# Kernel optimization log

Hardware: AMD Instinct MI355X
Metric: run time of the kernel (lower is better)

The kernel has to match this reference:

```python
import jax, jax.numpy as jnp
import numpy as np
import math

B, L, D = 4, 2048, 1024        # batch, x_len, x_dim
QKV, H = 64, 16                # qkv_dim, head_dim (number of heads)


def setup_inputs() -> dict:
    key = jax.random.key(0)
    ks = jax.random.split(key, 10)
    s = 1.0 / math.sqrt(D)
    return {
        "x": jax.random.normal(ks[0], (B, L, D), jnp.float32),
        "encoder_x": jax.random.normal(ks[1], (B, L, D), jnp.float32),
        "Wq": jax.random.normal(ks[2], (D, QKV * H), jnp.float32) * s,
        "bq": jax.random.normal(ks[3], (QKV * H,), jnp.float32) * 0.01,
        "Wk": jax.random.normal(ks[4], (D, QKV * H), jnp.float32) * s,
        "bk": jax.random.normal(ks[5], (QKV * H,), jnp.float32) * 0.01,
        "Wv": jax.random.normal(ks[6], (D, QKV * H), jnp.float32) * s,
        "bv": jax.random.normal(ks[7], (QKV * H,), jnp.float32) * 0.01,
        "Wo": jax.random.normal(ks[8], (QKV * H, D), jnp.float32) * s,
        "bo": jax.random.normal(ks[9], (D,), jnp.float32) * 0.01,
    }


def reference(x, encoder_x, Wq, bq, Wk, bk, Wv, bv, Wo, bo):
    # q,k from encoder_x; v from x  -> [B, L, H, QKV]
    q = (encoder_x @ Wq + bq).reshape(B, L, H, QKV)
    k = (encoder_x @ Wk + bk).reshape(B, L, H, QKV)
    v = (x @ Wv + bv).reshape(B, L, H, QKV)
    # explicit [B,H,L,L] score matrix + softmax over k (faithful to source)
    scores = jax.nn.softmax(
        jnp.einsum("bqhd,bkhd->bhqk", q, k) / math.sqrt(QKV), axis=-1
    )
    # faithful to source einsum 'bvhd,bhqk->bvhd': no shared contraction
    # index, so scores are summed over (q,k) and broadcast onto v per (b,h).
    attn = jnp.einsum("bvhd,bhqk->bvhd", v, scores).reshape(B, L, H * QKV)
    return attn @ Wo + bo
```

## Files before the change

### kernel.cpp

```cpp
#include <hip/hip_runtime.h>
#include <stdint.h>


typedef __attribute__((ext_vector_type(8))) short bf16x8;
typedef __attribute__((ext_vector_type(4))) float f32x4;

typedef __attribute__((address_space(1))) void as1_void;
typedef __attribute__((address_space(3))) void as3_void;
#define GLD16(g, s)                                                          \
  __builtin_amdgcn_global_load_lds((as1_void*)(g), (as3_void*)(s), 16, 0, 0)

__device__ __forceinline__ short f2bf(float f) {
  union { float f; uint32_t u; } v; v.f = f;
  uint32_t r = v.u + 0x7FFFu + ((v.u >> 16) & 1u);
  return (short)(r >> 16);
}

__device__ __forceinline__ bf16x8 pack8(f32x4 a, f32x4 b) {
  union { f32x4 f; uint32_t u[4]; } x, y;
  x.f = a; y.f = b;
#pragma unroll
  for (int t = 0; t < 4; ++t) x.u[t] += 0x8000u;
#pragma unroll
  for (int t = 0; t < 4; ++t) y.u[t] += 0x8000u;
  union { bf16x8 v; uint32_t u[4]; } o;
  o.u[0] = __builtin_amdgcn_perm(x.u[1], x.u[0], 0x07060302);
  o.u[1] = __builtin_amdgcn_perm(x.u[3], x.u[2], 0x07060302);
  o.u[2] = __builtin_amdgcn_perm(y.u[1], y.u[0], 0x07060302);
  o.u[3] = __builtin_amdgcn_perm(y.u[3], y.u[2], 0x07060302);
  return o.v;
}

__global__ __launch_bounds__(256) void mid(
    const float* __restrict__ Wo, const float* __restrict__ Wv,
    const float* __restrict__ bv, const float* __restrict__ bo,
    const float* __restrict__ x, short* __restrict__ x_bf,
    short* __restrict__ Wt, float* __restrict__ biasc) {
  constexpr int BK = 64, NW = 1024;
  __shared__ __align__(16) float Bsf[64 * BK];
  __shared__ __align__(16) float Ts[64 * 36];
  const int b = blockIdx.x, tid = threadIdx.x;

  if (b >= 576) {
    const int i = (b - 576) * 256 + tid;
    const float4* p = (const float4*)x;
    float4 a = p[2 * (size_t)i], c = p[2 * (size_t)i + 1];
    *(bf16x8*)(x_bf + 8 * (size_t)i) =
        pack8((f32x4){a.x, a.y, a.z, a.w}, (f32x4){c.x, c.y, c.z, c.w});
    return;
  }

  if (b >= 512) {
    float* red = Bsf;
    const int b3 = b - 512;
    const int nx = tid & 15, ky = tid >> 4;
    const int n = b3 * 16 + nx;
    float s = 0.f;
    for (int k = ky; k < 1024; k += 16)
      s += bv[k] * Wo[(size_t)k * NW + n];
    red[tid] = s;
    __syncthreads();
#pragma unroll
    for (int st = 128; st >= 16; st >>= 1) {
      if (tid < st) red[tid] += red[tid + st];
      __syncthreads();
    }
    if (ky == 0) biasc[n] = 2048.0f * red[nx] + bo[n];
    return;
  }

  const int lane = tid & 63, wave = tid >> 6;
  const int bm = (b >> 4) * 32, bn = (b & 15) * 64;
  const int wm = (wave & 1) * 16, wn = (wave >> 1) * 32;
  const int l15 = lane & 15, quad = lane >> 4;

  f32x4 acc[2];
  acc[0] = (f32x4){0.f, 0.f, 0.f, 0.f};
  acc[1] = (f32x4){0.f, 0.f, 0.f, 0.f};

  const int br = tid >> 4, bc4 = (tid & 15) ^ (br & 7);
  const float* pb = Wv + (size_t)(bn + br) * NW + bc4 * 4;
  float* lb = Bsf + tid * 4;

  const int ajr = tid >> 3, ac4 = (tid & 7) * 4;
  const float* pa = Wo + (size_t)ajr * NW + bm + ac4;

  for (int kt = 0; kt < 1024; kt += BK) {
    float4 va = *(const float4*)(pa);
    float4 vb = *(const float4*)(pa + 32 * (size_t)NW);
    pa += (size_t)BK * NW;
#pragma unroll
    for (int s = 0; s < 4; ++s) GLD16(pb + (size_t)(16 * s) * NW, lb + 1024 * s);
    pb += BK;
    *(float4*)(Ts + ajr * 36 + ac4) = va;
    *(float4*)(Ts + (ajr + 32) * 36 + ac4) = vb;
    __syncthreads();
#pragma unroll
    for (int kk = 0; kk < 2; ++kk) {
      const float* tsp = Ts + ((kk * 4 + quad) * 8) * 36 + wm + l15;
      float av[8];
#pragma unroll
      for (int e = 0; e < 8; ++e) av[e] = tsp[e * 36];
      bf16x8 af = pack8((f32x4){av[0], av[1], av[2], av[3]},
                        (f32x4){av[4], av[5], av[6], av[7]});
#pragma unroll
      for (int j = 0; j < 2; ++j) {
        const int rn = wn + j * 16 + l15;
        const int c4 = kk * 8 + quad * 2;
        f32x4 u0 = *(const f32x4*)(Bsf + (rn * 16 + (c4 ^ (rn & 7))) * 4);
        f32x4 u1 = *(const f32x4*)(Bsf + (rn * 16 + ((c4 + 1) ^ (rn & 7))) * 4);
        acc[j] = __builtin_amdgcn_mfma_f32_16x16x32_bf16(af, pack8(u0, u1),
                                                         acc[j], 0, 0, 0);
      }
    }
    __syncthreads();
  }
#pragma unroll
  for (int j = 0; j < 2; ++j) {
    const int col = bn + wn + j * 16 + l15;
    const int row0 = bm + wm + quad * 4;
#pragma unroll
    for (int r = 0; r < 4; ++r)
      Wt[(size_t)(row0 + r) * NW + col] = f2bf(2048.f * acc[j][r]);
  }
}

__global__ __launch_bounds__(256) void gemm_main(
    const short* __restrict__ A, const short* __restrict__ Bt,
    const float* __restrict__ bias, float* __restrict__ Out,
    int M, int N, int K) {
  constexpr int BK = 64;
  __shared__ __align__(16) char smem[65536];
  short* As0 = (short*)smem;
  short* Bs0 = (short*)(smem + 16384);
  short* As1 = (short*)(smem + 32768);
  short* Bs1 = (short*)(smem + 49152);
  const int tid = threadIdx.x, lane = tid & 63, wave = tid >> 6;
  const int b = blockIdx.x;
  const int bm = (b & 63) * 128;
  const int bn = (b >> 6) * 128;
  const int wm = (wave & 1) * 64, wn = (wave >> 1) * 64;
  const int l15 = lane & 15, quad = lane >> 4;

  f32x4 acc[4][4];
#pragma unroll
  for (int i = 0; i < 4; ++i)
#pragma unroll
    for (int j = 0; j < 4; ++j) acc[i][j] = (f32x4){0.f, 0.f, 0.f, 0.f};

  const int srow = tid >> 3, sc8 = (tid & 7) ^ (srow & 7);
  const short* pa = A + (size_t)(bm + srow) * K + sc8 * 8;
  const short* pb = Bt + (size_t)(bn + srow) * K + sc8 * 8;

#define STAGE(Asx, Bsx, kt)                                                  \
  {                                                                          \
    _Pragma("unroll") for (int s = 0; s < 4; ++s)                            \
        GLD16(pa + (size_t)(32 * s) * K + (kt), (Asx) + tid * 8 + 2048 * s); \
    _Pragma("unroll") for (int s = 0; s < 4; ++s)                            \
        GLD16(pb + (size_t)(32 * s) * K + (kt), (Bsx) + tid * 8 + 2048 * s); \
  }
#define COMPUTE(Asx, Bsx)                                                    \
  {                                                                          \
    _Pragma("unroll") for (int kk = 0; kk < 2; ++kk) {                       \
      bf16x8 af[4], bfr[4];                                                  \
      _Pragma("unroll") for (int i = 0; i < 4; ++i) {                        \
        const int r = wm + i * 16 + l15;                                     \
        af[i] = *(const bf16x8*)((Asx) + r * BK +                            \
                                 ((kk * 4 + quad) ^ (r & 7)) * 8);           \
      }                                                                      \
      _Pragma("unroll") for (int j = 0; j < 4; ++j) {                        \
        const int r = wn + j * 16 + l15;                                     \
        bfr[j] = *(const bf16x8*)((Bsx) + r * BK +                           \
                                  ((kk * 4 + quad) ^ (r & 7)) * 8);          \
      }                                                                      \
      _Pragma("unroll") for (int i = 0; i < 4; ++i)                          \
          _Pragma("unroll") for (int j = 0; j < 4; ++j)                      \
              acc[i][j] = __builtin_amdgcn_mfma_f32_16x16x32_bf16(           \
                  af[i], bfr[j], acc[i][j], 0, 0, 0);                        \
    }                                                                        \
  }

  STAGE(As0, Bs0, 0);
  __syncthreads();

  for (int trip = 0; trip < 8; ++trip) {
    const int kt_e = trip * 128;
    STAGE(As1, Bs1, kt_e + 64);
    COMPUTE(As0, Bs0);
    __syncthreads();
    if (trip < 7) {
      STAGE(As0, Bs0, kt_e + 128);
      COMPUTE(As1, Bs1);
      __syncthreads();
    } else {
      COMPUTE(As1, Bs1);
    }
  }
#undef STAGE
#undef COMPUTE

  float* T = (float*)smem + wave * 1088;
#pragma unroll
  for (int i = 0; i < 4; ++i) {
#pragma unroll
    for (int j = 0; j < 4; ++j) {
      const float bb = bias[bn + wn + j * 16 + l15];
#pragma unroll
      for (int r = 0; r < 4; ++r)
        T[(quad * 4 + r) * 68 + j * 16 + l15] = acc[i][j][r] + bb;
    }
#pragma unroll
    for (int p = 0; p < 4; ++p) {
      const int row = (lane >> 4) + 4 * p;
      const int ch = lane & 15;
      f32x4 v = *(const f32x4*)(T + row * 68 + ch * 4);
      *(f32x4*)(Out + (size_t)(bm + wm + i * 16 + row) * N + bn + wn +
                ch * 4) = v;
    }
  }
}

extern "C" void kernel_launch(void* const* d_in, const int* in_sizes, int n_in,
                              void* d_out, int out_size, void* d_ws,
                              size_t ws_size, hipStream_t stream) {
  const float* x  = (const float*)d_in[0];
  const float* Wv = (const float*)d_in[6];
  const float* bv = (const float*)d_in[7];
  const float* Wo = (const float*)d_in[8];
  const float* bo = (const float*)d_in[9];
  float* out = (float*)d_out;

  constexpr int D = 1024, NO = 1024;
  constexpr int M = 8192;

  char* ws = (char*)d_ws;
  short* x_bf  = (short*)(ws);
  short* wt_bf = (short*)(ws + (16u << 20));
  float* biasc = (float*)(ws + (18u << 20));

  mid<<<4672, 256, 0, stream>>>(Wo, Wv, bv, bo, x, x_bf, wt_bf, biasc);
  gemm_main<<<(M / 128) * (NO / 128), 256, 0, stream>>>(
      x_bf, wt_bf, biasc, out, M, NO, D);
}
```

Before: 153.9 us.

## Double-buffer LDS tiles in Wo·Wv precompute kernel to overlap loads with MFMA

The mid kernel's K-loop that forms the folded Wo·Wv weight now uses two LDS buffers for both operand tiles. The next tile's global loads and LDS stores are issued before the current tile's MFMA compute, and one barrier per step replaces two. This aims to hide global-load latency behind compute, at the cost of doubled LDS usage, which may reduce occupancy.

```diff
diff --git a/kernel.cpp b/kernel.cpp
--- a/kernel.cpp
+++ b/kernel.cpp
@@ -37,8 +37,10 @@
     const float* __restrict__ x, short* __restrict__ x_bf,
     short* __restrict__ Wt, float* __restrict__ biasc) {
   constexpr int BK = 64, NW = 1024;
-  __shared__ __align__(16) float Bsf[64 * BK];
-  __shared__ __align__(16) float Ts[64 * 36];
+  __shared__ __align__(16) float Bsf0[64 * BK];
+  __shared__ __align__(16) float Bsf1[64 * BK];
+  __shared__ __align__(16) float Ts0[64 * 36];
+  __shared__ __align__(16) float Ts1[64 * 36];
   const int b = blockIdx.x, tid = threadIdx.x;
 
   if (b >= 576) {
@@ -51,7 +53,7 @@
   }
 
   if (b >= 512) {
-    float* red = Bsf;
+    float* red = Bsf0;
     const int b3 = b - 512;
     const int nx = tid & 15, ky = tid >> 4;
     const int n = b3 * 16 + nx;
@@ -80,41 +82,57 @@
 
   const int br = tid >> 4, bc4 = (tid & 15) ^ (br & 7);
   const float* pb = Wv + (size_t)(bn + br) * NW + bc4 * 4;
-  float* lb = Bsf + tid * 4;
-
   const int ajr = tid >> 3, ac4 = (tid & 7) * 4;
   const float* pa = Wo + (size_t)ajr * NW + bm + ac4;
 
-  for (int kt = 0; kt < 1024; kt += BK) {
-    float4 va = *(const float4*)(pa);
-    float4 vb = *(const float4*)(pa + 32 * (size_t)NW);
-    pa += (size_t)BK * NW;
-#pragma unroll
-    for (int s = 0; s < 4; ++s) GLD16(pb + (size_t)(16 * s) * NW, lb + 1024 * s);
-    pb += BK;
-    *(float4*)(Ts + ajr * 36 + ac4) = va;
-    *(float4*)(Ts + (ajr + 32) * 36 + ac4) = vb;
+#define STAGEW(Tsx, Bsx, kt)                                                 \
+  {                                                                          \
+    float4 va = *(const float4*)(pa + (size_t)(kt)*NW);                      \
+    float4 vb = *(const float4*)(pa + (size_t)((kt) + 32) * NW);             \
+    _Pragma("unroll") for (int s = 0; s < 4; ++s)                            \
+        GLD16(pb + (size_t)(16 * s) * NW + (kt), (Bsx) + tid * 4 + 1024 * s);\
+    *(float4*)((Tsx) + ajr * 36 + ac4) = va;                                 \
+    *(float4*)((Tsx) + (ajr + 32) * 36 + ac4) = vb;                          \
+  }
+#define COMPW(Tsx, Bsx)                                                      \
+  {                                                                          \
+    _Pragma("unroll") for (int kk = 0; kk < 2; ++kk) {                       \
+      const float* tsp = (Tsx) + ((kk * 4 + quad) * 8) * 36 + wm + l15;      \
+      float av[8];                                                           \
+      _Pragma("unroll") for (int e = 0; e < 8; ++e) av[e] = tsp[e * 36];     \
+      bf16x8 af = pack8((f32x4){av[0], av[1], av[2], av[3]},                 \
+                        (f32x4){av[4], av[5], av[6], av[7]});                \
+      _Pragma("unroll") for (int j = 0; j < 2; ++j) {                        \
+        const int rn = wn + j * 16 + l15;                                    \
+        const int c4 = kk * 8 + quad * 2;                                    \
+        f32x4 u0 = *(const f32x4*)((Bsx) + (rn * 16 + (c4 ^ (rn & 7))) * 4); \
+        f32x4 u1 =                                                           \
+            *(const f32x4*)((Bsx) + (rn * 16 + ((c4 + 1) ^ (rn & 7))) * 4);  \
+        acc[j] = __builtin_amdgcn_mfma_f32_16x16x32_bf16(af, pack8(u0, u1),  \
+                                                         acc[j], 0, 0, 0);   \
+      }                                                                      \
+    }                                                                        \
+  }
+
+  STAGEW(Ts0, Bsf0, 0);
+  __syncthreads();
+
+  for (int trip = 0; trip < 8; ++trip) {
+    const int kt_e = trip * 128;
+    STAGEW(Ts1, Bsf1, kt_e + 64);
+    COMPW(Ts0, Bsf0);
     __syncthreads();
-#pragma unroll
-    for (int kk = 0; kk < 2; ++kk) {
-      const float* tsp = Ts + ((kk * 4 + quad) * 8) * 36 + wm + l15;
-      float av[8];
-#pragma unroll
-      for (int e = 0; e < 8; ++e) av[e] = tsp[e * 36];
-      bf16x8 af = pack8((f32x4){av[0], av[1], av[2], av[3]},
-                        (f32x4){av[4], av[5], av[6], av[7]});
-#pragma unroll
-      for (int j = 0; j < 2; ++j) {
-        const int rn = wn + j * 16 + l15;
-        const int c4 = kk * 8 + quad * 2;
-        f32x4 u0 = *(const f32x4*)(Bsf + (rn * 16 + (c4 ^ (rn & 7))) * 4);
-        f32x4 u1 = *(const f32x4*)(Bsf + (rn * 16 + ((c4 + 1) ^ (rn & 7))) * 4);
-        acc[j] = __builtin_amdgcn_mfma_f32_16x16x32_bf16(af, pack8(u0, u1),
-                                                         acc[j], 0, 0, 0);
-      }
-    }
-    __syncthreads();
-  }
+    if (trip < 7) {
+      STAGEW(Ts0, Bsf0, kt_e + 128);
+      COMPW(Ts1, Bsf1);
+      __syncthreads();
+    } else {
+      COMPW(Ts1, Bsf1);
+    }
+  }
+#undef STAGEW
+#undef COMPW
+
 #pragma unroll
   for (int j = 0; j < 2; ++j) {
     const int col = bn + wn + j * 16 + l15;
```

Result: faster. 150.7 us (-2.1%).
